# Kernel tuning notes

Hardware: AMD Instinct MI355X
Metric: run time of the kernel (lower is better)

The kernel has to match this reference:

```python
import jax, jax.numpy as jnp
import numpy as np

B, M, N, D, H = 8, 64, 64, 256, 8

def setup_inputs() -> dict:
    key = jax.random.key(0)
    kx, kq, kk, kv, ko = jax.random.split(key, 5)
    x = jax.random.normal(kx, (B, M, N, D), dtype=jnp.float32)
    q = jax.random.normal(kq, (H, D, D), dtype=jnp.float32)
    k = jax.random.normal(kk, (D, D), dtype=jnp.float32)
    v = jax.random.normal(kv, (D, D), dtype=jnp.float32)
    o = jax.random.normal(ko, (H, D, D), dtype=jnp.float32)
    return {"x": x, "q": q, "k": k, "v": v, "o": o}

def reference(x, q, k, v, o):
    # x: [b,m,n,d]; q,o: [h,d,d]; k,v: [d,d]
    Q = jnp.einsum('bmnd,hdk->bhmnk', x, q)      # [b,h,m,n,d]
    h_half = Q.shape[1] // 2
    Q1, Q2 = Q[:, :h_half], Q[:, h_half:]
    K = jnp.einsum('bmnd,dk->bmnk', x, k)        # [b,m,n,d]
    V = jnp.einsum('bmnd,dv->bmnv', x, v)        # [b,m,n,d]

    # Axis 1: attend along the m (row) axis for each column y
    logits1 = jnp.einsum('bhxyk,bzyk->bhyxz', Q1, K)   # [b,h/2,n,m,m]
    scores1 = jax.nn.softmax(logits1, axis=-1)
    O1 = jnp.einsum('bhyxz,bzyv->bhxyv', scores1, V)   # [b,h/2,m,n,d]

    # Axis 2: attend along the n (column) axis for each row x
    logits2 = jnp.einsum('bhxyk,bxzk->bhxyz', Q2, K)   # [b,h/2,m,n,n]
    scores2 = jax.nn.softmax(logits2, axis=-1)
    O2 = jnp.einsum('bhxyz,bxzv->bhxyv', scores2, V)   # [b,h/2,m,n,d]

    O = jnp.concatenate([O1, O2], axis=1)              # [b,h,m,n,d]
    # Faithful to original: 'bhmnd,hdv->bmnd' keeps d, sums over h and v
    Z = jnp.einsum('bhmnd,hdv->bmnd', O, o)
    return Z
```

## Files before the change

kernel.cpp:

```cpp
#include <hip/hip_runtime.h>

typedef unsigned short u16;
typedef __attribute__((ext_vector_type(8))) short short8;
typedef __attribute__((ext_vector_type(4))) float f32x4;

__device__ __forceinline__ float bf2f(u16 u){ return __uint_as_float(((unsigned)u)<<16); }
__device__ __forceinline__ u16 f2bf(float f){
  unsigned u = __float_as_uint(f);
  unsigned r = u + 0x7fffu + ((u>>16)&1u);
  return (u16)(r>>16);
}

#define MFMA16(a,b,c) __builtin_amdgcn_mfma_f32_16x16x32_bf16(a,b,c,0,0,0)

static constexpr int XS_STR  = 264;
static constexpr int PS_STR  = 72;
static constexpr int WT_STR  = 72;
static constexpr int XHI_OFF = 0;
static constexpr int XLO_OFF = 16896;
static constexpr int GHI_OFF = 33792;
static constexpr int GLO_OFF = 50688;
static constexpr int XVT_OFF = 33792;
static constexpr int PS_OFF  = 67584;
static constexpr int SMF_OFF = 72192;
static constexpr int SMEM_BYTES = (72192 + 512)*2;

static constexpr int MH_SMEM = 70656*2;


__global__ void prep_kernel(const float* __restrict__ k, const float* __restrict__ v,
                            const float* __restrict__ o, u16* __restrict__ khi,
                            u16* __restrict__ klo, u16* __restrict__ vT,
                            float* __restrict__ soP, float4* __restrict__ outz){
  __shared__ float Ts[64*65];
  const int blk = blockIdx.x, tid = threadIdx.x;
  if (blk < 64){
    int base = blk*1024 + tid*4;
    const float4 f4 = *(const float4*)(k + base);
    ushort4 hv, lv;
    hv.x=f2bf(f4.x); lv.x=f2bf(f4.x-bf2f(hv.x));
    hv.y=f2bf(f4.y); lv.y=f2bf(f4.y-bf2f(hv.y));
    hv.z=f2bf(f4.z); lv.z=f2bf(f4.z-bf2f(hv.z));
    hv.w=f2bf(f4.w); lv.w=f2bf(f4.w-bf2f(hv.w));
    *(ushort4*)&khi[base] = hv;
    *(ushort4*)&klo[base] = lv;
  } else if (blk < 80){
    int t = blk - 64;
    const int bi = (t>>2)<<6, bj = (t&3)<<6;
    #pragma unroll
    for (int p=0;p<4;p++){
      int idx4 = tid + (p<<8);
      int i = idx4 >> 4, c4 = (idx4 & 15) << 2;
      const float4 f4 = *(const float4*)(v + ((bi+i)<<8) + bj + c4);
      Ts[i*65+c4]=f4.x; Ts[i*65+c4+1]=f4.y; Ts[i*65+c4+2]=f4.z; Ts[i*65+c4+3]=f4.w;
    }
    __syncthreads();
    #pragma unroll
    for (int p=0;p<2;p++){
      int ch = tid + (p<<8);
      int j = ch >> 3, i8 = (ch & 7) << 3;
      short8 t8;
      #pragma unroll
      for (int e=0;e<8;e++) t8[e] = (short)f2bf(Ts[(i8+e)*65 + j]);
      *(short8*)&vT[((bj+j)<<8) + bi + i8] = t8;
    }
  } else if (blk < 336){
    int p = blk - 80;
    int h = p >> 5, base = (p & 31) << 3;
    int w = tid >> 6, l = tid & 63;
    #pragma unroll
    for (int i=0;i<2;i++){
      int row = base + w*2 + i;
      const float4 f4 = *(const float4*)(o + (((h<<8)+row)<<8) + (l<<2));
      float s = f4.x + f4.y + f4.z + f4.w;
      #pragma unroll
      for (int off=32; off>=1; off>>=1) s += __shfl_xor(s, off, 64);
      if (l==0) soP[(h<<8)+row] = s;
    }
  } else {
    int z = blk - 336;
    const float4 zf4 = {0.f,0.f,0.f,0.f};
    #pragma unroll
    for (int i=0;i<16;i++) outz[z*4096 + i*256 + tid] = zf4;
  }
}

__global__ __launch_bounds__(256,1) void mh_kernel(
    const float* __restrict__ q, const u16* __restrict__ khi,
    const u16* __restrict__ klo, u16* __restrict__ mhi, u16* __restrict__ mlo)
{
  extern __shared__ u16 sm[];
  u16* Qhi = sm;
  u16* Qlo = sm + 16896;
  u16* Chi = sm + 33792;
  u16* Clo = sm + 52224;

  const int tid = threadIdx.x;
  const int w = tid >> 6, lane = tid & 63;
  const int quad = lane >> 4, m16 = lane & 15;
  const int cw = w << 6, koq = quad << 3;
  const int h = blockIdx.x >> 2, dt = (blockIdx.x & 3) << 6;

  #pragma unroll
  for (int i=0;i<16;i++){
    int idx4 = i*256 + tid;
    int tr = idx4 >> 6, c4 = (idx4 & 63) << 2;
    const float4 xv = *(const float4*)(q + (((h<<8)+dt+tr)<<8) + c4);
    ushort4 hv, lv;
    hv.x=f2bf(xv.x); lv.x=f2bf(xv.x-bf2f(hv.x));
    hv.y=f2bf(xv.y); lv.y=f2bf(xv.y-bf2f(hv.y));
    hv.z=f2bf(xv.z); lv.z=f2bf(xv.z-bf2f(hv.z));
    hv.w=f2bf(xv.w); lv.w=f2bf(xv.w-bf2f(hv.w));
    *(ushort4*)&Qhi[tr*XS_STR + c4] = hv;
    *(ushort4*)&Qlo[tr*XS_STR + c4] = lv;
  }
  __syncthreads();

  const f32x4 zf = {0.f,0.f,0.f,0.f};
  f32x4 acc[4][4];
  #pragma unroll
  for (int r=0;r<4;r++)
    #pragma unroll
    for (int c=0;c<4;c++) acc[r][c] = zf;

  short8 Bh[2][4], Bl[2][4];
  #pragma unroll
  for (int c=0;c<4;c++){
    Bh[0][c] = *(const short8*)&khi[(cw + c*16 + m16)*256 + koq];
    Bl[0][c] = *(const short8*)&klo[(cw + c*16 + m16)*256 + koq];
  }
  #pragma unroll
  for (int kk=0;kk<8;kk++){
    const int cur = kk&1, nxt = cur^1;
    if (kk<7){
      const int ko2 = ((kk+1)<<5) + koq;
      #pragma unroll
      for (int c=0;c<4;c++){
        Bh[nxt][c] = *(const short8*)&khi[(cw + c*16 + m16)*256 + ko2];
        Bl[nxt][c] = *(const short8*)&klo[(cw + c*16 + m16)*256 + ko2];
      }
    }
    const int ko = (kk<<5) + koq;
    short8 Ah[4], Al[4];
    #pragma unroll
    for (int r=0;r<4;r++) Ah[r] = *(const short8*)&Qhi[(r*16+m16)*XS_STR + ko];
    #pragma unroll
    for (int r=0;r<4;r++) Al[r] = *(const short8*)&Qlo[(r*16+m16)*XS_STR + ko];
    #pragma unroll
    for (int r=0;r<4;r++)
      #pragma unroll
      for (int c=0;c<4;c++){
        acc[r][c] = MFMA16(Ah[r], Bh[cur][c], acc[r][c]);
        acc[r][c] = MFMA16(Ah[r], Bl[cur][c], acc[r][c]);
        acc[r][c] = MFMA16(Al[r], Bh[cur][c], acc[r][c]);
      }
  }

  #pragma unroll
  for (int r=0;r<4;r++)
    #pragma unroll
    for (int c=0;c<4;c++)
      #pragma unroll
      for (int g=0; g<4; g++){
        int drow = r*16 + quad*4 + g;
        int dp   = cw + c*16 + m16;
        float vv = acc[r][c][g];
        u16 hh = f2bf(vv);
        Chi[dp*WT_STR + drow] = hh;
        Clo[dp*WT_STR + drow] = f2bf(vv - bf2f(hh));
      }
  __syncthreads();

  #pragma unroll
  for (int p=0;p<8;p++){
    int ch = tid + (p<<8);
    int dp = ch >> 3, i8 = (ch & 7) << 3;
    *(int4*)&mhi[(((h<<8)+dp)<<8) + dt + i8] = *(const int4*)&Chi[dp*WT_STR + i8];
    *(int4*)&mlo[(((h<<8)+dp)<<8) + dt + i8] = *(const int4*)&Clo[dp*WT_STR + i8];
  }
}

__global__ __launch_bounds__(512,2) void attn_kernel(
    const float* __restrict__ x, const u16* __restrict__ mhiP,
    const u16* __restrict__ mloP, const u16* __restrict__ vT,
    const float* __restrict__ soP, float* __restrict__ out)
{
  extern __shared__ u16 sm[];
  u16* Xhi = sm + XHI_OFF;
  u16* Xlo = sm + XLO_OFF;
  u16* Ghi = sm + GHI_OFF;
  u16* Glo = sm + GLO_OFF;
  u16* Xvt = sm + XVT_OFF;
  u16* Ps  = sm + PS_OFF;
  float* SMf = (float*)(sm + SMF_OFF);

  const int tid  = threadIdx.x;
  const int w    = tid >> 6, lane = tid & 63;
  const int quad = lane >> 4, m16 = lane & 15;
  const int br   = blockIdx.x >> 9;
  const int idx  = blockIdx.x & 511;
  const int b    = idx >> 6, s = idx & 63;
  const int cw   = w << 5;
  const int rs   = (w >> 1) << 4;
  const int zh   = w & 1;
  const int koq  = quad << 3;

  auto tok = [&](int t)->int {
    int m = br ? s : t;
    int n = br ? t : s;
    return (((b<<6) + m) << 14) + (n << 8);
  };

  #pragma unroll
  for (int i=0;i<8;i++){
    int idx4 = i*512 + tid;
    int tr = idx4 >> 6, c4 = (idx4 & 63) << 2;
    const float4 xv = *(const float4*)(x + tok(tr) + c4);
    ushort4 hv, lv;
    hv.x=f2bf(xv.x); lv.x=f2bf(xv.x-bf2f(hv.x));
    hv.y=f2bf(xv.y); lv.y=f2bf(xv.y-bf2f(hv.y));
    hv.z=f2bf(xv.z); lv.z=f2bf(xv.z-bf2f(hv.z));
    hv.w=f2bf(xv.w); lv.w=f2bf(xv.w-bf2f(hv.w));
    *(ushort4*)&Xhi[tr*XS_STR + c4] = hv;
    *(ushort4*)&Xlo[tr*XS_STR + c4] = lv;
  }
  __syncthreads();

  const f32x4 zf = {0.f,0.f,0.f,0.f};
  f32x4 acc[4][2];

  {
    #pragma unroll
    for (int r=0;r<4;r++){ acc[r][0] = zf; acc[r][1] = zf; }
    #pragma unroll
    for (int kk=0;kk<8;kk++){
      const int ko = (kk<<5) + koq;
      short8 A[4], Bf[2];
      #pragma unroll
      for (int r=0;r<4;r++) A[r]  = *(const short8*)&Xhi[(r*16+m16)*XS_STR + ko];
      #pragma unroll
      for (int c=0;c<2;c++) Bf[c] = *(const short8*)&vT[(cw + c*16 + m16)*256 + ko];
      #pragma unroll
      for (int r=0;r<4;r++)
        #pragma unroll
        for (int c=0;c<2;c++) acc[r][c] = MFMA16(A[r], Bf[c], acc[r][c]);
    }
    #pragma unroll
    for (int r=0;r<4;r++)
      #pragma unroll
      for (int c=0;c<2;c++)
        #pragma unroll
        for (int g=0; g<4; g++){
          int z  = r*16 + quad*4 + g;
          int vc = cw + c*16 + m16;
          Xvt[vc*WT_STR + z] = f2bf(acc[r][c][g]);
        }
  }
  short8 XvB[2][2];
  #pragma unroll
  for (int kk=0;kk<2;kk++)
    #pragma unroll
    for (int c=0;c<2;c++)
      XvB[kk][c] = *(const short8*)&Xvt[(cw + c*16 + m16)*WT_STR + (kk<<5) + koq];
  __syncthreads();

  f32x4 Z[4][2];
  #pragma unroll
  for (int r=0;r<4;r++){ Z[r][0] = zf; Z[r][1] = zf; }

  for (int h=0; h<4; h++){
    const int gh = br*4 + h;
    const u16* __restrict__ Whi = mhiP + gh*65536;
    const u16* __restrict__ Wlo = mloP + gh*65536;

    #pragma unroll
    for (int r=0;r<4;r++){ acc[r][0] = zf; acc[r][1] = zf; }
    {
      short8 Bh[2][2], Bl[2][2];
      #pragma unroll
      for (int c=0;c<2;c++){
        Bh[0][c] = *(const short8*)&Whi[(cw + c*16 + m16)*256 + koq];
        Bl[0][c] = *(const short8*)&Wlo[(cw + c*16 + m16)*256 + koq];
      }
      #pragma unroll
      for (int kk=0;kk<8;kk++){
        const int cur = kk&1, nxt = cur^1;
        if (kk<7){
          const int ko2 = ((kk+1)<<5) + koq;
          #pragma unroll
          for (int c=0;c<2;c++){
            Bh[nxt][c] = *(const short8*)&Whi[(cw + c*16 + m16)*256 + ko2];
            Bl[nxt][c] = *(const short8*)&Wlo[(cw + c*16 + m16)*256 + ko2];
          }
        }
        const int ko = (kk<<5) + koq;
        short8 Ah[4], Al[4];
        #pragma unroll
        for (int r=0;r<4;r++) Ah[r] = *(const short8*)&Xhi[(r*16+m16)*XS_STR + ko];
        #pragma unroll
        for (int r=0;r<4;r++) Al[r] = *(const short8*)&Xlo[(r*16+m16)*XS_STR + ko];
        #pragma unroll
        for (int r=0;r<4;r++)
          #pragma unroll
          for (int c=0;c<2;c++){
            acc[r][c] = MFMA16(Ah[r], Bh[cur][c], acc[r][c]);
            acc[r][c] = MFMA16(Ah[r], Bl[cur][c], acc[r][c]);
            acc[r][c] = MFMA16(Al[r], Bh[cur][c], acc[r][c]);
          }
      }
    }
    #pragma unroll
    for (int r=0;r<4;r++)
      #pragma unroll
      for (int c=0;c<2;c++)
        #pragma unroll
        for (int g=0; g<4; g++){
          int row = r*16 + quad*4 + g;
          int col = cw + c*16 + m16;
          float vv = acc[r][c][g];
          u16 hh = f2bf(vv);
          Ghi[row*XS_STR + col] = hh;
          Glo[row*XS_STR + col] = f2bf(vv - bf2f(hh));
        }
    __syncthreads();

    f32x4 L[2];
    L[0] = zf; L[1] = zf;
    #pragma unroll
    for (int kk=0;kk<8;kk++){
      const int ko = (kk<<5) + koq;
      short8 Ahi = *(const short8*)&Ghi[(rs+m16)*XS_STR + ko];
      short8 Alo = *(const short8*)&Glo[(rs+m16)*XS_STR + ko];
      #pragma unroll
      for (int c=0;c<2;c++){
        short8 Bxh = *(const short8*)&Xhi[((zh<<5) + c*16 + m16)*XS_STR + ko];
        short8 Bxl = *(const short8*)&Xlo[((zh<<5) + c*16 + m16)*XS_STR + ko];
        L[c] = MFMA16(Ahi, Bxh, L[c]);
        L[c] = MFMA16(Ahi, Bxl, L[c]);
        L[c] = MFMA16(Alo, Bxh, L[c]);
      }
    }

    float mxl[4], sml[4];
    #pragma unroll
    for (int g=0; g<4; g++){
      float mx = fmaxf(L[0][g], L[1][g]);
      #pragma unroll
      for (int off=1; off<16; off<<=1) mx = fmaxf(mx, __shfl_xor(mx, off, 64));
      float sum = 0.f;
      #pragma unroll
      for (int c=0;c<2;c++){ float e = __expf(L[c][g]-mx); L[c][g] = e; sum += e; }
      #pragma unroll
      for (int off=1; off<16; off<<=1) sum += __shfl_xor(sum, off, 64);
      mxl[g] = mx; sml[g] = sum;
      if (m16 == 0){
        int row = rs + quad*4 + g;
        SMf[row*4 + zh*2]     = mx;
        SMf[row*4 + zh*2 + 1] = sum;
      }
    }
    __syncthreads();
    #pragma unroll
    for (int g=0; g<4; g++){
      int row = rs + quad*4 + g;
      float mxo = SMf[row*4 + (zh^1)*2];
      float smo = SMf[row*4 + (zh^1)*2 + 1];
      float M   = fmaxf(mxl[g], mxo);
      float al  = __expf(mxl[g]-M), ao = __expf(mxo-M);
      float scale = al / (sml[g]*al + smo*ao);
      #pragma unroll
      for (int c=0;c<2;c++)
        Ps[row*PS_STR + (zh<<5) + c*16 + m16] = f2bf(L[c][g]*scale);
    }
    __syncthreads();

    #pragma unroll
    for (int r=0;r<4;r++){ acc[r][0] = zf; acc[r][1] = zf; }
    #pragma unroll
    for (int kk=0;kk<2;kk++){
      const int ko = (kk<<5) + koq;
      short8 Ap[4];
      #pragma unroll
      for (int r=0;r<4;r++) Ap[r] = *(const short8*)&Ps[(r*16+m16)*PS_STR + ko];
      #pragma unroll
      for (int r=0;r<4;r++)
        #pragma unroll
        for (int c=0;c<2;c++) acc[r][c] = MFMA16(Ap[r], XvB[kk][c], acc[r][c]);
    }
    float sc[2];
    sc[0] = soP[gh*256 + cw + m16];
    sc[1] = soP[gh*256 + cw + 16 + m16];
    #pragma unroll
    for (int r=0;r<4;r++)
      #pragma unroll
      for (int c=0;c<2;c++)
        #pragma unroll
        for (int g=0; g<4; g++) Z[r][c][g] += sc[c]*acc[r][c][g];
  }

  #pragma unroll
  for (int r=0;r<4;r++)
    #pragma unroll
    for (int c=0;c<2;c++)
      #pragma unroll
      for (int g=0; g<4; g++){
        int t   = r*16 + quad*4 + g;
        int col = cw + c*16 + m16;
        atomicAdd(&out[tok(t) + col], Z[r][c][g]);
      }
}

extern "C" void kernel_launch(void* const* d_in, const int* in_sizes, int n_in,
                              void* d_out, int out_size, void* d_ws, size_t ws_size,
                              hipStream_t stream) {
  const float* x = (const float*)d_in[0];
  const float* q = (const float*)d_in[1];
  const float* k = (const float*)d_in[2];
  const float* v = (const float*)d_in[3];
  const float* o = (const float*)d_in[4];
  u16* ws   = (u16*)d_ws;
  u16* mhi  = ws;
  u16* mlo  = ws + 524288;
  u16* khi  = ws + 1048576;
  u16* klo  = ws + 1114112;
  u16* vT   = ws + 1179648;
  float* soP = (float*)(ws + 1245184);
  float* out = (float*)d_out;

  prep_kernel<<<848, 256, 0, stream>>>(k, v, o, khi, klo, vT, soP, (float4*)d_out);
  (void)hipFuncSetAttribute(reinterpret_cast<const void*>(&mh_kernel),
                            hipFuncAttributeMaxDynamicSharedMemorySize, MH_SMEM);
  mh_kernel<<<32, 256, MH_SMEM, stream>>>(q, khi, klo, mhi, mlo);

  (void)hipFuncSetAttribute(reinterpret_cast<const void*>(&attn_kernel),
                            hipFuncAttributeMaxDynamicSharedMemorySize, SMEM_BYTES);
  attn_kernel<<<1024, 512, SMEM_BYTES, stream>>>(x, mhi, mlo, vT, soP, out);
}
```

Baseline: 372.2 us.

## Shrink attention LDS footprint and fuse G-to-logits per tile to raise occupancy

The attention kernel no longer stores the full 64x256 G = X·M_h matrix (hi/lo) in shared memory. Each wave now computes 16x32 tiles of G and immediately folds them into the logits through a small per-wave scratch, and the two column-halves are reduced through LDS. This cuts the LDS footprint so four blocks can share a CU instead of two. The mh_kernel is split into 256 smaller blocks to fill more CUs. The trade-off is extra barriers, a serialized Xv transpose staging step, and more redundant LDS reads.

```diff
diff --git a/kernel.cpp b/kernel.cpp
--- a/kernel.cpp
+++ b/kernel.cpp
@@ -15,17 +15,12 @@
 
 static constexpr int XS_STR  = 264;
 static constexpr int PS_STR  = 72;
-static constexpr int WT_STR  = 72;
-static constexpr int XHI_OFF = 0;
 static constexpr int XLO_OFF = 16896;
-static constexpr int GHI_OFF = 33792;
-static constexpr int GLO_OFF = 50688;
-static constexpr int XVT_OFF = 33792;
-static constexpr int PS_OFF  = 67584;
-static constexpr int SMF_OFF = 72192;
-static constexpr int SMEM_BYTES = (72192 + 512)*2;
-
-static constexpr int MH_SMEM = 70656*2;
+static constexpr int R_OFF   = 33792;
+static constexpr int SMF_U16 = 38400;
+static constexpr int SMEM_BYTES = 38912*2;
+
+static constexpr int MH_SMEM = 22016*2;
 
 
 __global__ void prep_kernel(const float* __restrict__ k, const float* __restrict__ v,
@@ -91,18 +86,21 @@
 {
   extern __shared__ u16 sm[];
   u16* Qhi = sm;
-  u16* Qlo = sm + 16896;
-  u16* Chi = sm + 33792;
-  u16* Clo = sm + 52224;
+  u16* Qlo = sm + 8448;
+  u16* Chi = sm + 16896;
+  u16* Clo = sm + 19456;
 
   const int tid = threadIdx.x;
   const int w = tid >> 6, lane = tid & 63;
   const int quad = lane >> 4, m16 = lane & 15;
-  const int cw = w << 6, koq = quad << 3;
-  const int h = blockIdx.x >> 2, dt = (blockIdx.x & 3) << 6;
-
-  #pragma unroll
-  for (int i=0;i<16;i++){
+  const int cw2 = w << 4, koq = quad << 3;
+  const int h   = blockIdx.x >> 5;
+  const int rr  = blockIdx.x & 31;
+  const int dt  = (rr >> 2) << 5;
+  const int dpq = (rr & 3) << 6;
+
+  #pragma unroll
+  for (int i=0;i<8;i++){
     int idx4 = i*256 + tid;
     int tr = idx4 >> 6, c4 = (idx4 & 63) << 2;
     const float4 xv = *(const float4*)(q + (((h<<8)+dt+tr)<<8) + c4);
@@ -117,82 +115,49 @@
   __syncthreads();
 
   const f32x4 zf = {0.f,0.f,0.f,0.f};
-  f32x4 acc[4][4];
-  #pragma unroll
-  for (int r=0;r<4;r++)
-    #pragma unroll
-    for (int c=0;c<4;c++) acc[r][c] = zf;
-
-  short8 Bh[2][4], Bl[2][4];
-  #pragma unroll
-  for (int c=0;c<4;c++){
-    Bh[0][c] = *(const short8*)&khi[(cw + c*16 + m16)*256 + koq];
-    Bl[0][c] = *(const short8*)&klo[(cw + c*16 + m16)*256 + koq];
-  }
+  f32x4 a0 = zf, a1 = zf;
   #pragma unroll
   for (int kk=0;kk<8;kk++){
-    const int cur = kk&1, nxt = cur^1;
-    if (kk<7){
-      const int ko2 = ((kk+1)<<5) + koq;
-      #pragma unroll
-      for (int c=0;c<4;c++){
-        Bh[nxt][c] = *(const short8*)&khi[(cw + c*16 + m16)*256 + ko2];
-        Bl[nxt][c] = *(const short8*)&klo[(cw + c*16 + m16)*256 + ko2];
-      }
-    }
     const int ko = (kk<<5) + koq;
-    short8 Ah[4], Al[4];
-    #pragma unroll
-    for (int r=0;r<4;r++) Ah[r] = *(const short8*)&Qhi[(r*16+m16)*XS_STR + ko];
-    #pragma unroll
-    for (int r=0;r<4;r++) Al[r] = *(const short8*)&Qlo[(r*16+m16)*XS_STR + ko];
-    #pragma unroll
-    for (int r=0;r<4;r++)
-      #pragma unroll
-      for (int c=0;c<4;c++){
-        acc[r][c] = MFMA16(Ah[r], Bh[cur][c], acc[r][c]);
-        acc[r][c] = MFMA16(Ah[r], Bl[cur][c], acc[r][c]);
-        acc[r][c] = MFMA16(Al[r], Bh[cur][c], acc[r][c]);
-      }
-  }
-
-  #pragma unroll
-  for (int r=0;r<4;r++)
-    #pragma unroll
-    for (int c=0;c<4;c++)
-      #pragma unroll
-      for (int g=0; g<4; g++){
-        int drow = r*16 + quad*4 + g;
-        int dp   = cw + c*16 + m16;
-        float vv = acc[r][c][g];
-        u16 hh = f2bf(vv);
-        Chi[dp*WT_STR + drow] = hh;
-        Clo[dp*WT_STR + drow] = f2bf(vv - bf2f(hh));
-      }
+    short8 Ah0 = *(const short8*)&Qhi[(m16)*XS_STR + ko];
+    short8 Al0 = *(const short8*)&Qlo[(m16)*XS_STR + ko];
+    short8 Ah1 = *(const short8*)&Qhi[(16+m16)*XS_STR + ko];
+    short8 Al1 = *(const short8*)&Qlo[(16+m16)*XS_STR + ko];
+    short8 Bh  = *(const short8*)&khi[(dpq+cw2+m16)*256 + ko];
+    short8 Bl  = *(const short8*)&klo[(dpq+cw2+m16)*256 + ko];
+    a0 = MFMA16(Ah0,Bh,a0); a0 = MFMA16(Ah0,Bl,a0); a0 = MFMA16(Al0,Bh,a0);
+    a1 = MFMA16(Ah1,Bh,a1); a1 = MFMA16(Ah1,Bl,a1); a1 = MFMA16(Al1,Bh,a1);
+  }
+
+  const int dpl = cw2 + m16;
+  #pragma unroll
+  for (int g=0; g<4; g++){
+    float v0 = a0[g]; u16 h0 = f2bf(v0);
+    Chi[dpl*40 + quad*4+g] = h0;
+    Clo[dpl*40 + quad*4+g] = f2bf(v0 - bf2f(h0));
+    float v1 = a1[g]; u16 h1 = f2bf(v1);
+    Chi[dpl*40 + 16 + quad*4+g] = h1;
+    Clo[dpl*40 + 16 + quad*4+g] = f2bf(v1 - bf2f(h1));
+  }
   __syncthreads();
 
-  #pragma unroll
-  for (int p=0;p<8;p++){
-    int ch = tid + (p<<8);
-    int dp = ch >> 3, i8 = (ch & 7) << 3;
-    *(int4*)&mhi[(((h<<8)+dp)<<8) + dt + i8] = *(const int4*)&Chi[dp*WT_STR + i8];
-    *(int4*)&mlo[(((h<<8)+dp)<<8) + dt + i8] = *(const int4*)&Clo[dp*WT_STR + i8];
-  }
+  int dpo = tid >> 2, i8 = (tid & 3) << 3;
+  *(int4*)&mhi[(((h<<8)+dpq+dpo)<<8) + dt + i8] = *(const int4*)&Chi[dpo*40 + i8];
+  *(int4*)&mlo[(((h<<8)+dpq+dpo)<<8) + dt + i8] = *(const int4*)&Clo[dpo*40 + i8];
 }
 
-__global__ __launch_bounds__(512,2) void attn_kernel(
+__global__ __launch_bounds__(512,4) void attn_kernel(
     const float* __restrict__ x, const u16* __restrict__ mhiP,
     const u16* __restrict__ mloP, const u16* __restrict__ vT,
     const float* __restrict__ soP, float* __restrict__ out)
 {
   extern __shared__ u16 sm[];
-  u16* Xhi = sm + XHI_OFF;
+  u16* Xhi = sm;
   u16* Xlo = sm + XLO_OFF;
-  u16* Ghi = sm + GHI_OFF;
-  u16* Glo = sm + GLO_OFF;
-  u16* Xvt = sm + XVT_OFF;
-  u16* Ps  = sm + PS_OFF;
-  float* SMf = (float*)(sm + SMF_OFF);
+  u16* R   = sm + R_OFF;
+  u16* Ps  = R;
+  float* Rf  = (float*)R;
+  float* SMf = (float*)(sm + SMF_U16);
 
   const int tid  = threadIdx.x;
   const int w    = tid >> 6, lane = tid & 63;
@@ -201,9 +166,11 @@
   const int idx  = blockIdx.x & 511;
   const int b    = idx >> 6, s = idx & 63;
   const int cw   = w << 5;
-  const int rs   = (w >> 1) << 4;
-  const int zh   = w & 1;
+  const int rg   = w & 3;
+  const int cp   = w >> 2;
+  const int rs   = rg << 4;
   const int koq  = quad << 3;
+  u16* Rw = R + w*640;
 
   auto tok = [&](int t)->int {
     int m = br ? s : t;
@@ -227,155 +194,181 @@
   __syncthreads();
 
   const f32x4 zf = {0.f,0.f,0.f,0.f};
-  f32x4 acc[4][2];
-
-  {
-    #pragma unroll
-    for (int r=0;r<4;r++){ acc[r][0] = zf; acc[r][1] = zf; }
-    #pragma unroll
-    for (int kk=0;kk<8;kk++){
-      const int ko = (kk<<5) + koq;
-      short8 A[4], Bf[2];
-      #pragma unroll
-      for (int r=0;r<4;r++) A[r]  = *(const short8*)&Xhi[(r*16+m16)*XS_STR + ko];
-      #pragma unroll
-      for (int c=0;c<2;c++) Bf[c] = *(const short8*)&vT[(cw + c*16 + m16)*256 + ko];
+
+  f32x4 xacc[4][2];
+  #pragma unroll
+  for (int r=0;r<4;r++){ xacc[r][0] = zf; xacc[r][1] = zf; }
+  #pragma unroll
+  for (int kk=0;kk<8;kk++){
+    const int ko = (kk<<5) + koq;
+    short8 A[4], Bf[2];
+    #pragma unroll
+    for (int r=0;r<4;r++) A[r]  = *(const short8*)&Xhi[(r*16+m16)*XS_STR + ko];
+    #pragma unroll
+    for (int c=0;c<2;c++) Bf[c] = *(const short8*)&vT[(cw + c*16 + m16)*256 + ko];
+    #pragma unroll
+    for (int r=0;r<4;r++)
+      #pragma unroll
+      for (int c=0;c<2;c++) xacc[r][c] = MFMA16(A[r], Bf[c], xacc[r][c]);
+  }
+  short8 XvB[2][2];
+  for (int qq=0; qq<4; qq++){
+    if ((w>>1) == qq){
+      u16* slot = R + (w&1)*2304;
       #pragma unroll
       for (int r=0;r<4;r++)
         #pragma unroll
-        for (int c=0;c<2;c++) acc[r][c] = MFMA16(A[r], Bf[c], acc[r][c]);
-    }
-    #pragma unroll
-    for (int r=0;r<4;r++)
-      #pragma unroll
-      for (int c=0;c<2;c++)
+        for (int c=0;c<2;c++)
+          #pragma unroll
+          for (int g=0; g<4; g++)
+            slot[(c*16+m16)*72 + (r*16 + quad*4 + g)] = f2bf(xacc[r][c][g]);
+    }
+    __syncthreads();
+    if ((w>>1) == qq){
+      u16* slot = R + (w&1)*2304;
+      #pragma unroll
+      for (int kk=0;kk<2;kk++)
         #pragma unroll
-        for (int g=0; g<4; g++){
-          int z  = r*16 + quad*4 + g;
-          int vc = cw + c*16 + m16;
-          Xvt[vc*WT_STR + z] = f2bf(acc[r][c][g]);
+        for (int c=0;c<2;c++)
+          XvB[kk][c] = *(const short8*)&slot[(c*16+m16)*72 + (kk<<5) + koq];
+    }
+    __syncthreads();
+  }
+
+  f32x4 Z[4][2];
+  #pragma unroll
+  for (int r=0;r<4;r++){ Z[r][0] = zf; Z[r][1] = zf; }
+
+  for (int h=0; h<4; h++){
+    const int gh = (br<<2) + h;
+    const u16* __restrict__ Whi = mhiP + (gh<<16);
+    const u16* __restrict__ Wlo = mloP + (gh<<16);
+
+    f32x4 L0 = zf, L1 = zf, L2 = zf, L3 = zf;
+
+    #pragma unroll 1
+    for (int i=0; i<4; i++){
+      const int c = (i<<1) + cp;
+      const int cb32 = c << 5;
+      f32x4 a0 = zf, a1 = zf;
+      #pragma unroll
+      for (int kk=0;kk<8;kk++){
+        const int ko = (kk<<5) + koq;
+        short8 Ah = *(const short8*)&Xhi[(rs+m16)*XS_STR + ko];
+        short8 Al = *(const short8*)&Xlo[(rs+m16)*XS_STR + ko];
+        const u16* wp = Whi + (cb32+m16)*256 + ko;
+        const u16* lp = Wlo + (cb32+m16)*256 + ko;
+        short8 Bh0 = *(const short8*)wp;
+        short8 Bl0 = *(const short8*)lp;
+        short8 Bh1 = *(const short8*)(wp + 16*256);
+        short8 Bl1 = *(const short8*)(lp + 16*256);
+        a0 = MFMA16(Ah,Bh0,a0); a0 = MFMA16(Ah,Bl0,a0); a0 = MFMA16(Al,Bh0,a0);
+        a1 = MFMA16(Ah,Bh1,a1); a1 = MFMA16(Ah,Bl1,a1); a1 = MFMA16(Al,Bh1,a1);
+      }
+      #pragma unroll
+      for (int g=0; g<4; g++){
+        Rw[(quad*4+g)*40 + m16]      = f2bf(a0[g]);
+        Rw[(quad*4+g)*40 + 16 + m16] = f2bf(a1[g]);
+      }
+      short8 Ghi8 = *(const short8*)&Rw[m16*40 + koq];
+      const int dbase = cb32 + koq;
+      short8 Bxh0 = *(const short8*)&Xhi[(m16)*XS_STR + dbase];
+      short8 Bxh1 = *(const short8*)&Xhi[(16+m16)*XS_STR + dbase];
+      short8 Bxh2 = *(const short8*)&Xhi[(32+m16)*XS_STR + dbase];
+      short8 Bxh3 = *(const short8*)&Xhi[(48+m16)*XS_STR + dbase];
+      { short8 t = *(const short8*)&Xlo[(m16)*XS_STR + dbase];
+        L0 = MFMA16(Ghi8,Bxh0,L0); L0 = MFMA16(Ghi8,t,L0); }
+      { short8 t = *(const short8*)&Xlo[(16+m16)*XS_STR + dbase];
+        L1 = MFMA16(Ghi8,Bxh1,L1); L1 = MFMA16(Ghi8,t,L1); }
+      { short8 t = *(const short8*)&Xlo[(32+m16)*XS_STR + dbase];
+        L2 = MFMA16(Ghi8,Bxh2,L2); L2 = MFMA16(Ghi8,t,L2); }
+      { short8 t = *(const short8*)&Xlo[(48+m16)*XS_STR + dbase];
+        L3 = MFMA16(Ghi8,Bxh3,L3); L3 = MFMA16(Ghi8,t,L3); }
+      #pragma unroll
+      for (int g=0; g<4; g++){
+        float v0 = a0[g]; u16 h0 = f2bf(v0);
+        Rw[(quad*4+g)*40 + m16] = f2bf(v0 - bf2f(h0));
+        float v1 = a1[g]; u16 h1 = f2bf(v1);
+        Rw[(quad*4+g)*40 + 16 + m16] = f2bf(v1 - bf2f(h1));
+      }
+      short8 Glo8 = *(const short8*)&Rw[m16*40 + koq];
+      L0 = MFMA16(Glo8,Bxh0,L0);
+      L1 = MFMA16(Glo8,Bxh1,L1);
+      L2 = MFMA16(Glo8,Bxh2,L2);
+      L3 = MFMA16(Glo8,Bxh3,L3);
+    }
+    __syncthreads();
+
+    if (cp == 0){
+      #pragma unroll
+      for (int g=0; g<4; g++){
+        Rf[rg*512 +       (quad*4+g)*16 + m16] = L2[g];
+        Rf[rg*512 + 256 + (quad*4+g)*16 + m16] = L3[g];
+      }
+    }
+    __syncthreads();
+    if (cp == 1){
+      #pragma unroll
+      for (int g=0; g<4; g++){
+        L2[g] += Rf[rg*512 +       (quad*4+g)*16 + m16];
+        L3[g] += Rf[rg*512 + 256 + (quad*4+g)*16 + m16];
+      }
+      #pragma unroll
+      for (int g=0; g<4; g++){
+        Rf[rg*512 +       (quad*4+g)*16 + m16] = L0[g];
+        Rf[rg*512 + 256 + (quad*4+g)*16 + m16] = L1[g];
+      }
+    }
+    __syncthreads();
+    if (cp == 0){
+      #pragma unroll
+      for (int g=0; g<4; g++){
+        L0[g] += Rf[rg*512 +       (quad*4+g)*16 + m16];
+        L1[g] += Rf[rg*512 + 256 + (quad*4+g)*16 + m16];
+      }
+    }
+
+    float mxl[4], sml[4];
+    auto smLocal = [&](f32x4& La, f32x4& Lb){
+      #pragma unroll
+      for (int g=0; g<4; g++){
+        float mx = fmaxf(La[g], Lb[g]);
+        #pragma unroll
+        for (int off=1; off<16; off<<=1) mx = fmaxf(mx, __shfl_xor(mx, off, 64));
+        float e0 = __expf(La[g]-mx), e1 = __expf(Lb[g]-mx);
+        La[g] = e0; Lb[g] = e1;
+        float sum = e0 + e1;
+        #pragma unroll
+        for (int off=1; off<16; off<<=1) sum += __shfl_xor(sum, off, 64);
+        mxl[g] = mx; sml[g] = sum;
+        if (m16 == 0){
+          int row = rs + quad*4 + g;
+          SMf[row*4 + cp*2]     = mx;
+          SMf[row*4 + cp*2 + 1] = sum;
         }
-  }
-  short8 XvB[2][2];
-  #pragma unroll
-  for (int kk=0;kk<2;kk++)
-    #pragma unroll
-    for (int c=0;c<2;c++)
-      XvB[kk][c] = *(const short8*)&Xvt[(cw + c*16 + m16)*WT_STR + (kk<<5) + koq];
-  __syncthreads();
-
-  f32x4 Z[4][2];
-  #pragma unroll
-  for (int r=0;r<4;r++){ Z[r][0] = zf; Z[r][1] = zf; }
-
-  for (int h=0; h<4; h++){
-    const int gh = br*4 + h;
-    const u16* __restrict__ Whi = mhiP + gh*65536;
-    const u16* __restrict__ Wlo = mloP + gh*65536;
-
-    #pragma unroll
-    for (int r=0;r<4;r++){ acc[r][0] = zf; acc[r][1] = zf; }
-    {
-      short8 Bh[2][2], Bl[2][2];
-      #pragma unroll
-      for (int c=0;c<2;c++){
-        Bh[0][c] = *(const short8*)&Whi[(cw + c*16 + m16)*256 + koq];
-        Bl[0][c] = *(const short8*)&Wlo[(cw + c*16 + m16)*256 + koq];
-      }
-      #pragma unroll
-      for (int kk=0;kk<8;kk++){
-        const int cur = kk&1, nxt = cur^1;
-        if (kk<7){
-          const int ko2 = ((kk+1)<<5) + koq;
-          #pragma unroll
-          for (int c=0;c<2;c++){
-            Bh[nxt][c] = *(const short8*)&Whi[(cw + c*16 + m16)*256 + ko2];
-            Bl[nxt][c] = *(const short8*)&Wlo[(cw + c*16 + m16)*256 + ko2];
-          }
-        }
-        const int ko = (kk<<5) + koq;
-        short8 Ah[4], Al[4];
-        #pragma unroll
-        for (int r=0;r<4;r++) Ah[r] = *(const short8*)&Xhi[(r*16+m16)*XS_STR + ko];
-        #pragma unroll
-        for (int r=0;r<4;r++) Al[r] = *(const short8*)&Xlo[(r*16+m16)*XS_STR + ko];
-        #pragma unroll
-        for (int r=0;r<4;r++)
-          #pragma unroll
-          for (int c=0;c<2;c++){
-            acc[r][c] = MFMA16(Ah[r], Bh[cur][c], acc[r][c]);
-            acc[r][c] = MFMA16(Ah[r], Bl[cur][c], acc[r][c]);
-            acc[r][c] = MFMA16(Al[r], Bh[cur][c], acc[r][c]);
-          }
-      }
-    }
-    #pragma unroll
-    for (int r=0;r<4;r++)
-      #pragma unroll
-      for (int c=0;c<2;c++)
-        #pragma unroll
-        for (int g=0; g<4; g++){
-          int row = r*16 + quad*4 + g;
-          int col = cw + c*16 + m16;
-          float vv = acc[r][c][g];
-          u16 hh = f2bf(vv);
-          Ghi[row*XS_STR + col] = hh;
-          Glo[row*XS_STR + col] = f2bf(vv - bf2f(hh));
-        }
-    __syncthreads();
-
-    f32x4 L[2];
-    L[0] = zf; L[1] = zf;
-    #pragma unroll
-    for (int kk=0;kk<8;kk++){
-      const int ko = (kk<<5) + koq;
-      short8 Ahi = *(const short8*)&Ghi[(rs+m16)*XS_STR + ko];
-      short8 Alo = *(const short8*)&Glo[(rs+m16)*XS_STR + ko];
-      #pragma unroll
-      for (int c=0;c<2;c++){
-        short8 Bxh = *(const short8*)&Xhi[((zh<<5) + c*16 + m16)*XS_STR + ko];
-        short8 Bxl = *(const short8*)&Xlo[((zh<<5) + c*16 + m16)*XS_STR + ko];
-        L[c] = MFMA16(Ahi, Bxh, L[c]);
-        L[c] = MFMA16(Ahi, Bxl, L[c]);
-        L[c] = MFMA16(Alo, Bxh, L[c]);
-      }
-    }
-
-    float mxl[4], sml[4];
-    #pragma unroll
-    for (int g=0; g<4; g++){
-      float mx = fmaxf(L[0][g], L[1][g]);
-      #pragma unroll
-      for (int off=1; off<16; off<<=1) mx = fmaxf(mx, __shfl_xor(mx, off, 64));
-      float sum = 0.f;
-      #pragma unroll
-      for (int c=0;c<2;c++){ float e = __expf(L[c][g]-mx); L[c][g] = e; sum += e; }
-      #pragma unroll
-      for (int off=1; off<16; off<<=1) sum += __shfl_xor(sum, off, 64);
-      mxl[g] = mx; sml[g] = sum;
-      if (m16 == 0){
+      }
+    };
+    if (cp == 0) smLocal(L0, L1); else smLocal(L2, L3);
+    __syncthreads();
+    auto psW = [&](f32x4& La, f32x4& Lb){
+      #pragma unroll
+      for (int g=0; g<4; g++){
         int row = rs + quad*4 + g;
-        SMf[row*4 + zh*2]     = mx;
-        SMf[row*4 + zh*2 + 1] = sum;
-      }
-    }
-    __syncthreads();
-    #pragma unroll
-    for (int g=0; g<4; g++){
-      int row = rs + quad*4 + g;
-      float mxo = SMf[row*4 + (zh^1)*2];
-      float smo = SMf[row*4 + (zh^1)*2 + 1];
-      float M   = fmaxf(mxl[g], mxo);
-      float al  = __expf(mxl[g]-M), ao = __expf(mxo-M);
-      float scale = al / (sml[g]*al + smo*ao);
-      #pragma unroll
-      for (int c=0;c<2;c++)
-        Ps[row*PS_STR + (zh<<5) + c*16 + m16] = f2bf(L[c][g]*scale);
-    }
-    __syncthreads();
-
-    #pragma unroll
-    for (int r=0;r<4;r++){ acc[r][0] = zf; acc[r][1] = zf; }
+        float mxo = SMf[row*4 + (cp^1)*2];
+        float smo = SMf[row*4 + (cp^1)*2 + 1];
+        float M   = fmaxf(mxl[g], mxo);
+        float al  = __expf(mxl[g]-M), ao = __expf(mxo-M);
+        float scale = al / (sml[g]*al + smo*ao);
+        Ps[row*PS_STR + (cp<<5) + m16]      = f2bf(La[g]*scale);
+        Ps[row*PS_STR + (cp<<5) + 16 + m16] = f2bf(Lb[g]*scale);
+      }
+    };
+    if (cp == 0) psW(L0, L1); else psW(L2, L3);
+    __syncthreads();
+
+    f32x4 ya[4][2];
+    #pragma unroll
+    for (int r=0;r<4;r++){ ya[r][0] = zf; ya[r][1] = zf; }
     #pragma unroll
     for (int kk=0;kk<2;kk++){
       const int ko = (kk<<5) + koq;
@@ -385,17 +378,18 @@
       #pragma unroll
       for (int r=0;r<4;r++)
         #pragma unroll
-        for (int c=0;c<2;c++) acc[r][c] = MFMA16(Ap[r], XvB[kk][c], acc[r][c]);
-    }
-    float sc[2];
-    sc[0] = soP[gh*256 + cw + m16];
-    sc[1] = soP[gh*256 + cw + 16 + m16];
+        for (int c=0;c<2;c++) ya[r][c] = MFMA16(Ap[r], XvB[kk][c], ya[r][c]);
+    }
+    float sc0 = soP[gh*256 + cw + m16];
+    float sc1 = soP[gh*256 + cw + 16 + m16];
     #pragma unroll
     for (int r=0;r<4;r++)
       #pragma unroll
-      for (int c=0;c<2;c++)
-        #pragma unroll
-        for (int g=0; g<4; g++) Z[r][c][g] += sc[c]*acc[r][c][g];
+      for (int g=0; g<4; g++){
+        Z[r][0][g] += sc0*ya[r][0][g];
+        Z[r][1][g] += sc1*ya[r][1][g];
+      }
+    __syncthreads();
   }
 
   #pragma unroll
@@ -430,7 +424,7 @@
   prep_kernel<<<848, 256, 0, stream>>>(k, v, o, khi, klo, vT, soP, (float4*)d_out);
   (void)hipFuncSetAttribute(reinterpret_cast<const void*>(&mh_kernel),
                             hipFuncAttributeMaxDynamicSharedMemorySize, MH_SMEM);
-  mh_kernel<<<32, 256, MH_SMEM, stream>>>(q, khi, klo, mhi, mlo);
+  mh_kernel<<<256, 256, MH_SMEM, stream>>>(q, khi, klo, mhi, mlo);
 
   (void)hipFuncSetAttribute(reinterpret_cast<const void*>(&attn_kernel),
                             hipFuncAttributeMaxDynamicSharedMemorySize, SMEM_BYTES);
```

After: 630.9 us. +69.5%, slower.
